# Performance work log

Hardware: AMD Instinct MI355X
Metric: run time of the kernel (lower is better)

## Reference

```python
import jax, jax.numpy as jnp
import numpy as np

NUM_HEAD = 8


def setup_inputs() -> dict:
    key = jax.random.key(0)
    k1, k2, k3, k4 = jax.random.split(key, 4)
    B, C, H, W = 16, 512, 64, 64
    x = jax.random.normal(k1, (B, C, H, W), dtype=jnp.float32)
    w_qkv = jax.random.normal(k2, (3 * C, C), dtype=jnp.float32) * 0.02  # Conv2d 1x1, no bias
    w_proj = jax.random.normal(k3, (C, C), dtype=jnp.float32) * 0.02
    b_proj = jax.random.normal(k4, (C,), dtype=jnp.float32) * 0.02
    return {"x": x, "w_qkv": w_qkv, "w_proj": w_proj, "b_proj": b_proj}


def reference(x, w_qkv, w_proj, b_proj):
    B, C, H, W = x.shape
    nh = NUM_HEAD
    hd = C // nh
    scale = hd ** (-0.5)
    # 1x1 conv == channel matmul
    qkv = jnp.einsum('oc,bchw->bohw', w_qkv, x)  # [B, 3C, H, W]
    q, k, v = jnp.split(qkv, 3, axis=1)
    q = q.reshape(B, nh, hd, H * W)
    k = k.reshape(B, nh, hd, H * W)
    v = v.reshape(B, nh, hd, H * W)
    # NOTE: faithful to source: contracts over the spatial (last) axis,
    # producing a [B, nh, hd, hd] matrix.
    attn = jnp.einsum('bnqd,bnkd->bnqk', q, k) * scale
    attn = jax.nn.softmax(attn, axis=-1)
    # Faithful to source: 'k' and 'v' are both summed independently (outer sum),
    # exactly as torch.einsum computes it.
    out = jnp.einsum('bnqk,bnvd->bnqd', attn, v)
    out = out.reshape(B, C, H, W)
    return jnp.einsum('oc,bchw->bohw', w_proj, out) + b_proj[None, :, None, None]
```

## Files before the change

kernel.cpp:

```cpp
#include <hip/hip_runtime.h>

#define CDIM 512
#define NH 8
#define HWDIM 4096
#define TILE 128
#define NT 512

__global__ __launch_bounds__(256) void prep_kernel(
    const float* __restrict__ wqkv, const float* __restrict__ wproj,
    float* __restrict__ wvT, float* __restrict__ wp) {
  int idx = blockIdx.x * 256 + threadIdx.x;
  if (idx < 4096) {
    int c = idx >> 3, n = idx & 7;
    const float* p = wqkv + (size_t)(1024 + n * 64) * CDIM + c;
    float s = 0.f;
#pragma unroll 8
    for (int j = 0; j < 64; ++j) s += p[(size_t)j * CDIM];
    wvT[idx] = s;
  } else if (idx < 8192) {
    int i2 = idx - 4096;
    int o = i2 >> 3, n = i2 & 7;
    const float* p = wproj + (size_t)o * CDIM + n * 64;
    float s = 0.f;
#pragma unroll 8
    for (int j = 0; j < 64; ++j) s += p[j];
    wp[i2] = s;
  }
}

__global__ __launch_bounds__(NT, 4) void fused_kernel(
    const float* __restrict__ x, const float* __restrict__ bias,
    const float* __restrict__ wvT, const float* __restrict__ wp,
    float* __restrict__ y) {
  __shared__ __align__(16) float sWv[4096];
  __shared__ __align__(16) float sWp[4096];
  __shared__ __align__(16) float sB[512];
  __shared__ __align__(16) float sS[8][NH][TILE];

  const int t = threadIdx.x;
  for (int i = t; i < 4096; i += NT) { sWv[i] = wvT[i]; sWp[i] = wp[i]; }
  if (t < 512) sB[t] = bias[t];
  __syncthreads();

  const int wave = t >> 6;
  const int lane = t & 63;
  const int pos0 = blockIdx.x * TILE;
  const int b = pos0 >> 12;
  const int hw0 = pos0 & (HWDIM - 1);
  const float* xb = x + ((size_t)b * CDIM) * HWDIM + hw0 + lane * 2;

  float acc[NH][2];
#pragma unroll
  for (int n = 0; n < NH; ++n) { acc[n][0] = 0.f; acc[n][1] = 0.f; }

  const int c0 = wave * 64;
#pragma unroll 8
  for (int cc = 0; cc < 64; ++cc) {
    const int c = c0 + cc;
    const float2 xv = *(const float2*)(xb + (size_t)c * HWDIM);
    const float4 w0 = *(const float4*)&sWv[c * 8];
    const float4 w1 = *(const float4*)&sWv[c * 8 + 4];
    const float wn[8] = {w0.x, w0.y, w0.z, w0.w, w1.x, w1.y, w1.z, w1.w};
#pragma unroll
    for (int n = 0; n < NH; ++n) {
      acc[n][0] = fmaf(wn[n], xv.x, acc[n][0]);
      acc[n][1] = fmaf(wn[n], xv.y, acc[n][1]);
    }
  }

#pragma unroll
  for (int n = 0; n < NH; ++n) {
    *(float2*)&sS[wave][n][lane * 2] = make_float2(acc[n][0], acc[n][1]);
  }
  __syncthreads();

  float S2[NH][2];
#pragma unroll
  for (int n = 0; n < NH; ++n) {
    float s0 = 0.f, s1 = 0.f;
#pragma unroll
    for (int w = 0; w < 8; ++w) {
      const float2 a = *(const float2*)&sS[w][n][lane * 2];
      s0 += a.x; s1 += a.y;
    }
    S2[n][0] = s0; S2[n][1] = s1;
  }

  float* yb = y + ((size_t)b * CDIM) * HWDIM + hw0 + lane * 2;
  const int o0 = wave * 64;
#pragma unroll 4
  for (int oo = 0; oo < 64; ++oo) {
    const int o = o0 + oo;
    const float4 w0 = *(const float4*)&sWp[o * 8];
    const float4 w1 = *(const float4*)&sWp[o * 8 + 4];
    const float wn[8] = {w0.x, w0.y, w0.z, w0.w, w1.x, w1.y, w1.z, w1.w};
    const float bb = sB[o];
    float r0 = bb, r1 = bb;
#pragma unroll
    for (int n = 0; n < NH; ++n) {
      r0 = fmaf(wn[n], S2[n][0], r0);
      r1 = fmaf(wn[n], S2[n][1], r1);
    }
    *(float2*)(yb + (size_t)o * HWDIM) = make_float2(r0, r1);
  }
}

extern "C" void kernel_launch(void* const* d_in, const int* in_sizes, int n_in,
                              void* d_out, int out_size, void* d_ws, size_t ws_size,
                              hipStream_t stream) {
  const float* x     = (const float*)d_in[0];
  const float* wqkv  = (const float*)d_in[1];
  const float* wproj = (const float*)d_in[2];
  const float* bproj = (const float*)d_in[3];
  float* y = (float*)d_out;

  float* wvT = (float*)d_ws;
  float* wp  = wvT + 4096;

  prep_kernel<<<32, 256, 0, stream>>>(wqkv, wproj, wvT, wp);
  fused_kernel<<<HWDIM * 16 / TILE, NT, 0, stream>>>(x, bproj, wvT, wp, y);
}
```

Baseline: 259.0 us.

## Software-pipeline x reads with y writes across position tiles per block

Each block now handles four 64-position tiles in sequence. The projection and store of one tile is interleaved with the reduction loads of the next, and a double-buffered shared partial-sum array separates the tiles. Channel order is rotated per block so concurrent blocks touch different rows, and output writes become nontemporal stores. This is meant to keep read and write traffic overlapped and to amortize the per-block weight load into shared memory. In exchange it uses fewer blocks, scalar rather than float2 accesses, and a lower occupancy hint in the launch bounds.

New measurement: 260.3 us. No clear change (+0.5%).

```diff
diff --git a/kernel.cpp b/kernel.cpp
--- a/kernel.cpp
+++ b/kernel.cpp
@@ -3,7 +3,8 @@
 #define CDIM 512
 #define NH 8
 #define HWDIM 4096
-#define TILE 128
+#define TPOS 64
+#define NTILE 4
 #define NT 512
 
 __global__ __launch_bounds__(256) void prep_kernel(
@@ -28,14 +29,14 @@
   }
 }
 
-__global__ __launch_bounds__(NT, 4) void fused_kernel(
+__global__ __launch_bounds__(NT, 1) void fused_kernel(
     const float* __restrict__ x, const float* __restrict__ bias,
     const float* __restrict__ wvT, const float* __restrict__ wp,
     float* __restrict__ y) {
   __shared__ __align__(16) float sWv[4096];
   __shared__ __align__(16) float sWp[4096];
   __shared__ __align__(16) float sB[512];
-  __shared__ __align__(16) float sS[8][NH][TILE];
+  __shared__ __align__(16) float sS[2][8][NH][TPOS];
 
   const int t = threadIdx.x;
   for (int i = t; i < 4096; i += NT) { sWv[i] = wvT[i]; sWp[i] = wp[i]; }
@@ -44,64 +45,95 @@
 
   const int wave = t >> 6;
   const int lane = t & 63;
-  const int pos0 = blockIdx.x * TILE;
+  const int pos0 = blockIdx.x * (NTILE * TPOS);
   const int b = pos0 >> 12;
   const int hw0 = pos0 & (HWDIM - 1);
-  const float* xb = x + ((size_t)b * CDIM) * HWDIM + hw0 + lane * 2;
+  const float* xb = x + ((size_t)b * CDIM) * HWDIM + hw0 + lane;
+  float* yb = y + ((size_t)b * CDIM) * HWDIM + hw0 + lane;
 
-  float acc[NH][2];
+  const int g0 = wave * 64;
+  const int rot  = (blockIdx.x * 37) & 63;
+  const int rot2 = (blockIdx.x * 23) & 63;
+
+  float S2[NH];
+  float acc[NH];
+
 #pragma unroll
-  for (int n = 0; n < NH; ++n) { acc[n][0] = 0.f; acc[n][1] = 0.f; }
-
-  const int c0 = wave * 64;
+  for (int n = 0; n < NH; ++n) acc[n] = 0.f;
 #pragma unroll 8
-  for (int cc = 0; cc < 64; ++cc) {
-    const int c = c0 + cc;
-    const float2 xv = *(const float2*)(xb + (size_t)c * HWDIM);
+  for (int i = 0; i < 64; ++i) {
+    const int c = g0 + ((i + rot) & 63);
+    const float xv = xb[(size_t)c * HWDIM];
     const float4 w0 = *(const float4*)&sWv[c * 8];
     const float4 w1 = *(const float4*)&sWv[c * 8 + 4];
-    const float wn[8] = {w0.x, w0.y, w0.z, w0.w, w1.x, w1.y, w1.z, w1.w};
+    acc[0] = fmaf(w0.x, xv, acc[0]); acc[1] = fmaf(w0.y, xv, acc[1]);
+    acc[2] = fmaf(w0.z, xv, acc[2]); acc[3] = fmaf(w0.w, xv, acc[3]);
+    acc[4] = fmaf(w1.x, xv, acc[4]); acc[5] = fmaf(w1.y, xv, acc[5]);
+    acc[6] = fmaf(w1.z, xv, acc[6]); acc[7] = fmaf(w1.w, xv, acc[7]);
+  }
+#pragma unroll
+  for (int n = 0; n < NH; ++n) sS[0][wave][n][lane] = acc[n];
+  __syncthreads();
+#pragma unroll
+  for (int n = 0; n < NH; ++n) {
+    float s = 0.f;
+#pragma unroll
+    for (int w = 0; w < 8; ++w) s += sS[0][w][n][lane];
+    S2[n] = s;
+  }
+
+  for (int tt = 1; tt < NTILE; ++tt) {
+    const float* xbt = xb + tt * TPOS;
+    float* ybp = yb + (tt - 1) * TPOS;
+#pragma unroll
+    for (int n = 0; n < NH; ++n) acc[n] = 0.f;
+#pragma unroll 8
+    for (int i = 0; i < 64; ++i) {
+      const int o = g0 + ((i + rot2) & 63);
+      const float4 p0 = *(const float4*)&sWp[o * 8];
+      const float4 p1 = *(const float4*)&sWp[o * 8 + 4];
+      float r = sB[o];
+      r = fmaf(p0.x, S2[0], r); r = fmaf(p0.y, S2[1], r);
+      r = fmaf(p0.z, S2[2], r); r = fmaf(p0.w, S2[3], r);
+      r = fmaf(p1.x, S2[4], r); r = fmaf(p1.y, S2[5], r);
+      r = fmaf(p1.z, S2[6], r); r = fmaf(p1.w, S2[7], r);
+      __builtin_nontemporal_store(r, ybp + (size_t)o * HWDIM);
+      const int c = g0 + ((i + rot) & 63);
+      const float xv = xbt[(size_t)c * HWDIM];
+      const float4 w0 = *(const float4*)&sWv[c * 8];
+      const float4 w1 = *(const float4*)&sWv[c * 8 + 4];
+      acc[0] = fmaf(w0.x, xv, acc[0]); acc[1] = fmaf(w0.y, xv, acc[1]);
+      acc[2] = fmaf(w0.z, xv, acc[2]); acc[3] = fmaf(w0.w, xv, acc[3]);
+      acc[4] = fmaf(w1.x, xv, acc[4]); acc[5] = fmaf(w1.y, xv, acc[5]);
+      acc[6] = fmaf(w1.z, xv, acc[6]); acc[7] = fmaf(w1.w, xv, acc[7]);
+    }
+    const int buf = tt & 1;
+#pragma unroll
+    for (int n = 0; n < NH; ++n) sS[buf][wave][n][lane] = acc[n];
+    __syncthreads();
 #pragma unroll
     for (int n = 0; n < NH; ++n) {
-      acc[n][0] = fmaf(wn[n], xv.x, acc[n][0]);
-      acc[n][1] = fmaf(wn[n], xv.y, acc[n][1]);
+      float s = 0.f;
+#pragma unroll
+      for (int w = 0; w < 8; ++w) s += sS[buf][w][n][lane];
+      S2[n] = s;
     }
   }
 
-#pragma unroll
-  for (int n = 0; n < NH; ++n) {
-    *(float2*)&sS[wave][n][lane * 2] = make_float2(acc[n][0], acc[n][1]);
-  }
-  __syncthreads();
-
-  float S2[NH][2];
-#pragma unroll
-  for (int n = 0; n < NH; ++n) {
-    float s0 = 0.f, s1 = 0.f;
-#pragma unroll
-    for (int w = 0; w < 8; ++w) {
-      const float2 a = *(const float2*)&sS[w][n][lane * 2];
-      s0 += a.x; s1 += a.y;
+  {
+    float* ybp = yb + (NTILE - 1) * TPOS;
+#pragma unroll 8
+    for (int i = 0; i < 64; ++i) {
+      const int o = g0 + ((i + rot2) & 63);
+      const float4 p0 = *(const float4*)&sWp[o * 8];
+      const float4 p1 = *(const float4*)&sWp[o * 8 + 4];
+      float r = sB[o];
+      r = fmaf(p0.x, S2[0], r); r = fmaf(p0.y, S2[1], r);
+      r = fmaf(p0.z, S2[2], r); r = fmaf(p0.w, S2[3], r);
+      r = fmaf(p1.x, S2[4], r); r = fmaf(p1.y, S2[5], r);
+      r = fmaf(p1.z, S2[6], r); r = fmaf(p1.w, S2[7], r);
+      __builtin_nontemporal_store(r, ybp + (size_t)o * HWDIM);
     }
-    S2[n][0] = s0; S2[n][1] = s1;
-  }
-
-  float* yb = y + ((size_t)b * CDIM) * HWDIM + hw0 + lane * 2;
-  const int o0 = wave * 64;
-#pragma unroll 4
-  for (int oo = 0; oo < 64; ++oo) {
-    const int o = o0 + oo;
-    const float4 w0 = *(const float4*)&sWp[o * 8];
-    const float4 w1 = *(const float4*)&sWp[o * 8 + 4];
-    const float wn[8] = {w0.x, w0.y, w0.z, w0.w, w1.x, w1.y, w1.z, w1.w};
-    const float bb = sB[o];
-    float r0 = bb, r1 = bb;
-#pragma unroll
-    for (int n = 0; n < NH; ++n) {
-      r0 = fmaf(wn[n], S2[n][0], r0);
-      r1 = fmaf(wn[n], S2[n][1], r1);
-    }
-    *(float2*)(yb + (size_t)o * HWDIM) = make_float2(r0, r1);
   }
 }
 
@@ -118,5 +150,5 @@
   float* wp  = wvT + 4096;
 
   prep_kernel<<<32, 256, 0, stream>>>(wqkv, wproj, wvT, wp);
-  fused_kernel<<<HWDIM * 16 / TILE, NT, 0, stream>>>(x, bproj, wvT, wp, y);
+  fused_kernel<<<(16 * HWDIM) / (NTILE * TPOS), NT, 0, stream>>>(x, bproj, wvT, wp, y);
 }
```

## Widen tile to 256 positions with float4 loads, batched prefetch, nontemporal stores

Applied to the files above, without the earlier changes.

Each block now covers 256 spatial positions, so every lane handles 4 columns and uses 128-bit loads and stores. The channel loop loads 16 x vectors ahead before the FMAs to keep more memory requests in flight, and the output is written with nontemporal stores so it does not pollute the cache. Launch bounds drop to one block per CU, which raises the register budget but halves the grid to 256 blocks, leaving fewer waves to hide latency on a streaming, bandwidth-bound kernel.

Measured after the change: 245.3 us. 1.06x faster.

```diff
diff --git a/kernel.cpp b/kernel.cpp
--- a/kernel.cpp
+++ b/kernel.cpp
@@ -3,8 +3,10 @@
 #define CDIM 512
 #define NH 8
 #define HWDIM 4096
-#define TILE 128
+#define TILE 256
 #define NT 512
+
+typedef float f32x4 __attribute__((ext_vector_type(4)));
 
 __global__ __launch_bounds__(256) void prep_kernel(
     const float* __restrict__ wqkv, const float* __restrict__ wproj,
@@ -28,7 +30,7 @@
   }
 }
 
-__global__ __launch_bounds__(NT, 4) void fused_kernel(
+__global__ __launch_bounds__(NT, 1) void fused_kernel(
     const float* __restrict__ x, const float* __restrict__ bias,
     const float* __restrict__ wvT, const float* __restrict__ wp,
     float* __restrict__ y) {
@@ -47,46 +49,53 @@
   const int pos0 = blockIdx.x * TILE;
   const int b = pos0 >> 12;
   const int hw0 = pos0 & (HWDIM - 1);
-  const float* xb = x + ((size_t)b * CDIM) * HWDIM + hw0 + lane * 2;
+  const float* xb = x + ((size_t)b * CDIM) * HWDIM + hw0 + lane * 4;
 
-  float acc[NH][2];
+  float acc[NH][4];
 #pragma unroll
-  for (int n = 0; n < NH; ++n) { acc[n][0] = 0.f; acc[n][1] = 0.f; }
+  for (int n = 0; n < NH; ++n) { acc[n][0] = acc[n][1] = acc[n][2] = acc[n][3] = 0.f; }
 
   const int c0 = wave * 64;
-#pragma unroll 8
-  for (int cc = 0; cc < 64; ++cc) {
-    const int c = c0 + cc;
-    const float2 xv = *(const float2*)(xb + (size_t)c * HWDIM);
-    const float4 w0 = *(const float4*)&sWv[c * 8];
-    const float4 w1 = *(const float4*)&sWv[c * 8 + 4];
-    const float wn[8] = {w0.x, w0.y, w0.z, w0.w, w1.x, w1.y, w1.z, w1.w};
+  for (int g = 0; g < 4; ++g) {
+    float4 xv[16];
 #pragma unroll
-    for (int n = 0; n < NH; ++n) {
-      acc[n][0] = fmaf(wn[n], xv.x, acc[n][0]);
-      acc[n][1] = fmaf(wn[n], xv.y, acc[n][1]);
+    for (int j = 0; j < 16; ++j)
+      xv[j] = *(const float4*)(xb + (size_t)(c0 + g * 16 + j) * HWDIM);
+#pragma unroll
+    for (int j = 0; j < 16; ++j) {
+      const int c = c0 + g * 16 + j;
+      const float4 w0 = *(const float4*)&sWv[c * 8];
+      const float4 w1 = *(const float4*)&sWv[c * 8 + 4];
+      const float wn[8] = {w0.x, w0.y, w0.z, w0.w, w1.x, w1.y, w1.z, w1.w};
+      const float xr[4] = {xv[j].x, xv[j].y, xv[j].z, xv[j].w};
+#pragma unroll
+      for (int n = 0; n < NH; ++n) {
+#pragma unroll
+        for (int p = 0; p < 4; ++p) acc[n][p] = fmaf(wn[n], xr[p], acc[n][p]);
+      }
     }
   }
 
 #pragma unroll
   for (int n = 0; n < NH; ++n) {
-    *(float2*)&sS[wave][n][lane * 2] = make_float2(acc[n][0], acc[n][1]);
+    *(float4*)&sS[wave][n][lane * 4] =
+        make_float4(acc[n][0], acc[n][1], acc[n][2], acc[n][3]);
   }
   __syncthreads();
 
-  float S2[NH][2];
+  float S4[NH][4];
 #pragma unroll
   for (int n = 0; n < NH; ++n) {
-    float s0 = 0.f, s1 = 0.f;
+    float s0 = 0.f, s1 = 0.f, s2 = 0.f, s3 = 0.f;
 #pragma unroll
     for (int w = 0; w < 8; ++w) {
-      const float2 a = *(const float2*)&sS[w][n][lane * 2];
-      s0 += a.x; s1 += a.y;
+      const float4 a = *(const float4*)&sS[w][n][lane * 4];
+      s0 += a.x; s1 += a.y; s2 += a.z; s3 += a.w;
     }
-    S2[n][0] = s0; S2[n][1] = s1;
+    S4[n][0] = s0; S4[n][1] = s1; S4[n][2] = s2; S4[n][3] = s3;
   }
 
-  float* yb = y + ((size_t)b * CDIM) * HWDIM + hw0 + lane * 2;
+  float* yb = y + ((size_t)b * CDIM) * HWDIM + hw0 + lane * 4;
   const int o0 = wave * 64;
 #pragma unroll 4
   for (int oo = 0; oo < 64; ++oo) {
@@ -95,13 +104,16 @@
     const float4 w1 = *(const float4*)&sWp[o * 8 + 4];
     const float wn[8] = {w0.x, w0.y, w0.z, w0.w, w1.x, w1.y, w1.z, w1.w};
     const float bb = sB[o];
-    float r0 = bb, r1 = bb;
+    f32x4 r;
+    r.x = bb; r.y = bb; r.z = bb; r.w = bb;
 #pragma unroll
     for (int n = 0; n < NH; ++n) {
-      r0 = fmaf(wn[n], S2[n][0], r0);
-      r1 = fmaf(wn[n], S2[n][1], r1);
+      r.x = fmaf(wn[n], S4[n][0], r.x);
+      r.y = fmaf(wn[n], S4[n][1], r.y);
+      r.z = fmaf(wn[n], S4[n][2], r.z);
+      r.w = fmaf(wn[n], S4[n][3], r.w);
     }
-    *(float2*)(yb + (size_t)o * HWDIM) = make_float2(r0, r1);
+    __builtin_nontemporal_store(r, (f32x4*)(yb + (size_t)o * HWDIM));
   }
 }
 
@@ -118,5 +130,5 @@
   float* wp  = wvT + 4096;
 
   prep_kernel<<<32, 256, 0, stream>>>(wqkv, wproj, wvT, wp);
-  fused_kernel<<<HWDIM * 16 / TILE, NT, 0, stream>>>(x, bproj, wvT, wp, y);
+  fused_kernel<<<(16 * HWDIM) / TILE, NT, 0, stream>>>(x, bproj, wvT, wp, y);
 }
```
